# Performance work log

Hardware: AMD Instinct MI355X
Metric: run time of the kernel (lower is better)

Reference implementation:

```python
import jax, jax.numpy as jnp
import numpy as np

EPS = 1e-12  # F.normalize default eps


def setup_inputs() -> dict:
    key = jax.random.key(0)
    k1, k2, k3 = jax.random.split(key, 3)
    B, C, H, W = 4, 64, 64, 64
    background = jax.random.normal(k1, (B, C, H, W), dtype=jnp.float32)
    foreground = jax.random.normal(k2, (B, C, H, W), dtype=jnp.float32)
    # binary mask, broadcast over channels
    mask = jnp.round(jax.random.uniform(k3, (B, 1, H, W), dtype=jnp.float32))
    return {"background": background, "foreground": foreground, "mask": mask}


def _l2norm(x, axis):
    # matches torch F.normalize: x / max(||x||, eps)
    n = jnp.sqrt(jnp.sum(x * x, axis=axis, keepdims=True))
    return x / jnp.maximum(n, EPS)


def reference(background, foreground, mask):
    B, C, H, W = background.shape
    bg_flat = background.reshape(B, C, H * W)   # [B, C, K]
    fg_flat = foreground.reshape(B, C, H * W)   # [B, C, Q]
    norm_bg = _l2norm(bg_flat, axis=1)
    norm_fg = _l2norm(fg_flat, axis=1)
    # cosine-similarity scores [B, K, Q]
    attention = jnp.einsum('bck,bcq->bkq', norm_bg, norm_fg)
    attention = jax.nn.softmax(attention, axis=1)  # over bg (key) axis
    attended = jnp.einsum('bck,bkq->bcq', bg_flat, attention)
    attended = attended.reshape(B, C, H, W)
    return foreground * (1.0 - mask) + attended * mask
```

## Files before the change

kernel.cpp:

```cpp
#include <hip/hip_runtime.h>
#include <math.h>

#define CC 64
#define HWN 4096
#define QB 64
#define KSPLIT 8
#define KT 32
#define NITER (HWN / KSPLIT / KT)
#define NKC (HWN / KT)

typedef __attribute__((ext_vector_type(8))) short bf16x8;
typedef __attribute__((ext_vector_type(4))) float f32x4;

__device__ __align__(16) unsigned short g_bgT[4][HWN][CC];
__device__ __align__(16) unsigned short g_bgN[4][NKC][CC][KT];
__device__ __align__(16) unsigned short g_fgT[4][HWN][CC];

static __device__ __forceinline__ unsigned int f2bf(float x) {
  union { float f; unsigned int u; } v; v.f = x;
  return (v.u + 0x7fffu + ((v.u >> 16) & 1u)) >> 16;
}
static __device__ __forceinline__ unsigned int packbf(float lo, float hi) {
  return f2bf(lo) | (f2bf(hi) << 16);
}

__global__ __launch_bounds__(256) void prep_kernel(const float* __restrict__ bg,
                                                   const float* __restrict__ fg) {
  __shared__ float lds[64 * 65];
  const int bid = blockIdx.x;
  const int kt = bid & 63, b = (bid >> 6) & 3, which = bid >> 8;
  const float* src = (which ? fg : bg) + (size_t)b * CC * HWN + kt * 64;
  const int tid = threadIdx.x;

  {
    int c = tid >> 2, k0 = (tid & 3) * 16;
#pragma unroll
    for (int j4 = 0; j4 < 4; ++j4) {
      float4 v = *(const float4*)(src + (size_t)c * HWN + k0 + 4 * j4);
      lds[(k0 + 4 * j4 + 0) * 65 + c] = v.x;
      lds[(k0 + 4 * j4 + 1) * 65 + c] = v.y;
      lds[(k0 + 4 * j4 + 2) * 65 + c] = v.z;
      lds[(k0 + 4 * j4 + 3) * 65 + c] = v.w;
    }
  }
  __syncthreads();

  const int k = tid >> 2, u = tid & 3;
  float ss = 0.f;
#pragma unroll
  for (int j = 0; j < 16; ++j) {
    float v = lds[k * 65 + u * 16 + j];
    ss = fmaf(v, v, ss);
  }
  ss += __shfl_xor(ss, 1, 64);
  ss += __shfl_xor(ss, 2, 64);
  const float s = 1.0f / fmaxf(sqrtf(ss), 1e-12f);

  {
    unsigned int* gT32 = (unsigned int*)(which ? &g_fgT[0][0][0] : &g_bgT[0][0][0]);
    size_t R = (size_t)b * HWN + kt * 64 + k;
    unsigned int w8[8];
#pragma unroll
    for (int i = 0; i < 8; ++i) {
      int c2 = u * 16 + 2 * i;
      w8[i] = packbf(lds[k * 65 + c2] * s, lds[k * 65 + c2 + 1] * s);
    }
    *(uint4*)&gT32[R * 32 + u * 8]     = make_uint4(w8[0], w8[1], w8[2], w8[3]);
    *(uint4*)&gT32[R * 32 + u * 8 + 4] = make_uint4(w8[4], w8[5], w8[6], w8[7]);
  }

  if (which == 0) {
    unsigned int* gN32 = (unsigned int*)&g_bgN[0][0][0][0];
    int cN = tid >> 2, vN = tid & 3;
    unsigned int n8[8];
#pragma unroll
    for (int i = 0; i < 8; ++i) {
      int kk = vN * 16 + 2 * i;
      n8[i] = packbf(lds[kk * 65 + cN], lds[(kk + 1) * 65 + cN]);
    }
    int kc = kt * 2 + (vN >> 1);
    size_t RN = (((size_t)b * NKC + kc) * CC + cN) * (KT / 2) + (vN & 1) * 8;
    *(uint4*)&gN32[RN]     = make_uint4(n8[0], n8[1], n8[2], n8[3]);
    *(uint4*)&gN32[RN + 4] = make_uint4(n8[4], n8[5], n8[6], n8[7]);
  }
}

#define P_OFF 65536
#define ML_OFF 106496
#define SMEM_BYTES 108544
__global__ __launch_bounds__(512, 2) void attn_kernel(const float* __restrict__ fg,
                                                      const float* __restrict__ mask,
                                                      float* __restrict__ out) {
  __shared__ __align__(16) char smem[SMEM_BYTES];
  const int wg = blockIdx.x;
  const int wgp = (wg & 7) * 32 + (wg >> 3);
  const int b = wgp >> 6;
  const int q0 = (wgp & 63) * QB;
  const int tid = threadIdx.x;
  const int lane = tid & 63;
  const int ks = tid >> 6;
  const int m16 = lane & 15;
  const int quad = lane >> 4;

  bf16x8 Bf[4][2];
#pragma unroll
  for (int qf = 0; qf < 4; ++qf)
#pragma unroll
    for (int h = 0; h < 2; ++h)
      Bf[qf][h] = *(const bf16x8*)&g_fgT[b][q0 + qf * 16 + m16][h * 32 + quad * 8];

  const unsigned short* srcT[4];
#pragma unroll
  for (int t = 0; t < 4; ++t) {
    int uT = t * 64 + lane;
    int kk = uT >> 3, pos = uT & 7, j = pos ^ (kk & 7);
    srcT[t] = &g_bgT[b][ks * 512 + kk][j * 8];
  }

  const unsigned short* pN = &g_bgN[b][ks * 16][m16][quad * 8];

  unsigned short* P = (unsigned short*)(smem + P_OFF + ks * 5120);
  float* mL = (float*)(smem + ML_OFF);

  float l_run[4] = {0.f, 0.f, 0.f, 0.f};
  f32x4 O[4][4];
#pragma unroll
  for (int t = 0; t < 4; ++t)
#pragma unroll
    for (int qf = 0; qf < 4; ++qf) O[t][qf] = (f32x4){0.f, 0.f, 0.f, 0.f};

  char* const myT = smem + ks * 8192;

  auto stageT = [&](int bufsel) {
#pragma unroll
    for (int t = 0; t < 4; ++t) {
      __builtin_amdgcn_global_load_lds(
          (const __attribute__((address_space(1))) unsigned int*)srcT[t],
          (__attribute__((address_space(3))) unsigned int*)(myT + bufsel * 4096 + t * 1024),
          16, 0, 0);
      srcT[t] += KT * CC;
    }
  };

  bf16x8 A0r[4], A1r[4];
  auto loadN = [&](bf16x8 (&A)[4], int ch) {
#pragma unroll
    for (int t = 0; t < 4; ++t)
      A[t] = *(const bf16x8*)(pN + (size_t)ch * (CC * KT) + t * 16 * KT);
  };

  auto iter = [&](int it, int co, bf16x8 (&Ac)[4], bf16x8 (&An)[4]) {
    if (it + 1 < NITER) {
      stageT(co ^ 1);
      loadN(An, it + 1);
      asm volatile("s_waitcnt vmcnt(8)" ::: "memory");
    } else {
      asm volatile("s_waitcnt vmcnt(0)" ::: "memory");
    }

    const char* baseT = myT + co * 4096;

    f32x4 S[4][2];
    __builtin_amdgcn_s_setprio(1);
#pragma unroll
    for (int i = 0; i < 2; ++i) {
      int kk = 16 * i + m16;
      bf16x8 T0 = *(const bf16x8*)(baseT + kk * 128 + ((quad) ^ (kk & 7)) * 16);
      bf16x8 T1 = *(const bf16x8*)(baseT + kk * 128 + ((4 + quad) ^ (kk & 7)) * 16);
#pragma unroll
      for (int qf = 0; qf < 4; ++qf) {
        f32x4 acc = {0.f, 0.f, 0.f, 0.f};
        acc = __builtin_amdgcn_mfma_f32_16x16x32_bf16(T0, Bf[qf][0], acc, 0, 0, 0);
        acc = __builtin_amdgcn_mfma_f32_16x16x32_bf16(T1, Bf[qf][1], acc, 0, 0, 0);
        S[qf][i] = acc;
      }
    }
    __builtin_amdgcn_s_setprio(0);

#pragma unroll
    for (int qf = 0; qf < 4; ++qf)
#pragma unroll
      for (int i = 0; i < 2; ++i) {
        float pe[4];
#pragma unroll
        for (int r = 0; r < 4; ++r) {
          pe[r] = __expf(S[qf][i][r] - 1.0f);
          l_run[qf] += pe[r];
        }
        union { float f; unsigned int u; } x0, x1, x2, x3;
        x0.f = pe[0]; x1.f = pe[1]; x2.f = pe[2]; x3.f = pe[3];
        unsigned int p01 = __builtin_amdgcn_perm(x1.u + 0x8000u, x0.u + 0x8000u, 0x07060302u);
        unsigned int p23 = __builtin_amdgcn_perm(x3.u + 0x8000u, x2.u + 0x8000u, 0x07060302u);
        *(uint2*)&P[(qf * 16 + m16) * 40 + 16 * i + quad * 4] = make_uint2(p01, p23);
      }

    bf16x8 Pf[4];
#pragma unroll
    for (int qf = 0; qf < 4; ++qf)
      Pf[qf] = *(const bf16x8*)&P[(qf * 16 + m16) * 40 + quad * 8];
    __builtin_amdgcn_s_setprio(1);
#pragma unroll
    for (int t = 0; t < 4; ++t)
#pragma unroll
      for (int qf = 0; qf < 4; ++qf)
        O[t][qf] = __builtin_amdgcn_mfma_f32_16x16x32_bf16(Ac[t], Pf[qf], O[t][qf], 0, 0, 0);
    __builtin_amdgcn_s_setprio(0);
  };

  stageT(0);
  loadN(A0r, 0);

  for (int it2 = 0; it2 < NITER; it2 += 2) {
    iter(it2,     0, A0r, A1r);
    iter(it2 + 1, 1, A1r, A0r);
  }

#pragma unroll
  for (int qf = 0; qf < 4; ++qf) {
    l_run[qf] += __shfl_xor(l_run[qf], 16, 64);
    l_run[qf] += __shfl_xor(l_run[qf], 32, 64);
  }
  if (quad == 0) {
#pragma unroll
    for (int qf = 0; qf < 4; ++qf) mL[ks * 64 + qf * 16 + m16] = l_run[qf];
  }
  float* mO = (float*)smem;
  const float* fgB = fg + (size_t)b * CC * HWN;
  const float* mk = mask + (size_t)b * HWN;
  float* outB = out + (size_t)b * CC * HWN;

#pragma unroll
  for (int half = 0; half < 2; ++half) {
    __syncthreads();
#pragma unroll
    for (int qh = 0; qh < 2; ++qh) {
      int qf = half * 2 + qh;
#pragma unroll
      for (int t = 0; t < 4; ++t)
#pragma unroll
        for (int r = 0; r < 4; ++r)
          mO[(ks * 64 + 16 * t + quad * 4 + r) * 34 + qh * 16 + m16] = O[t][qf][r];
    }
    __syncthreads();
    {
      int q = tid & 31, cb = tid >> 5;
      int qglob = q0 + half * 32 + q;
      float L = 0.f;
#pragma unroll
      for (int s = 0; s < 8; ++s) L += mL[s * 64 + half * 32 + q];
      float invL = 1.0f / L;
      float mv = mk[qglob];
#pragma unroll
      for (int e = 0; e < 4; ++e) {
        int c = cb * 4 + e;
        float acc = 0.f;
#pragma unroll
        for (int s = 0; s < 8; ++s) acc += mO[(s * 64 + c) * 34 + q];
        float att = acc * invL;
        float fgv = fgB[(size_t)c * HWN + qglob];
        outB[(size_t)c * HWN + qglob] = fgv + mv * (att - fgv);
      }
    }
  }
}

extern "C" void kernel_launch(void* const* d_in, const int* in_sizes, int n_in,
                              void* d_out, int out_size, void* d_ws, size_t ws_size,
                              hipStream_t stream) {
  const float* background = (const float*)d_in[0];
  const float* foreground = (const float*)d_in[1];
  const float* mask       = (const float*)d_in[2];
  float* out = (float*)d_out;
  prep_kernel<<<512, 256, 0, stream>>>(background, foreground);
  attn_kernel<<<dim3(HWN / QB * 4), 512, 0, stream>>>(foreground, mask, out);
}
```

Baseline: 91.74 us.

## Keep P in registers via 16x16x16 MFMA and load bg tiles directly from global

The softmax probabilities stay in registers and are fed straight into 16x16x16 bf16 MFMAs, whose operand layout matches the score accumulator layout. This removes the LDS round trip for P. The background score tiles are now loaded from global memory into registers instead of being staged into LDS with global_load_lds, and the LDS footprint shrinks. The cost is twice as many MFMA instructions for the PV product, at half the K depth each, plus more register pressure and more outstanding global loads per iteration.

```diff
diff --git a/kernel.cpp b/kernel.cpp
--- a/kernel.cpp
+++ b/kernel.cpp
@@ -10,6 +10,7 @@
 #define NKC (HWN / KT)
 
 typedef __attribute__((ext_vector_type(8))) short bf16x8;
+typedef __attribute__((ext_vector_type(4))) short bf16x4;
 typedef __attribute__((ext_vector_type(4))) float f32x4;
 
 __device__ __align__(16) unsigned short g_bgT[4][HWN][CC];
@@ -85,9 +86,8 @@
   }
 }
 
-#define P_OFF 65536
-#define ML_OFF 106496
-#define SMEM_BYTES 108544
+#define ML_OFF 69632
+#define SMEM_BYTES 71680
 __global__ __launch_bounds__(512, 2) void attn_kernel(const float* __restrict__ fg,
                                                       const float* __restrict__ mask,
                                                       float* __restrict__ out) {
@@ -109,17 +109,9 @@
     for (int h = 0; h < 2; ++h)
       Bf[qf][h] = *(const bf16x8*)&g_fgT[b][q0 + qf * 16 + m16][h * 32 + quad * 8];
 
-  const unsigned short* srcT[4];
-#pragma unroll
-  for (int t = 0; t < 4; ++t) {
-    int uT = t * 64 + lane;
-    int kk = uT >> 3, pos = uT & 7, j = pos ^ (kk & 7);
-    srcT[t] = &g_bgT[b][ks * 512 + kk][j * 8];
-  }
-
-  const unsigned short* pN = &g_bgN[b][ks * 16][m16][quad * 8];
-
-  unsigned short* P = (unsigned short*)(smem + P_OFF + ks * 5120);
+  const unsigned short* const baseT = &g_bgT[b][ks * 512][0];
+  const unsigned short* const baseN = &g_bgN[b][ks * 16][0][0];
+
   float* mL = (float*)(smem + ML_OFF);
 
   float l_run[4] = {0.f, 0.f, 0.f, 0.f};
@@ -129,54 +121,50 @@
 #pragma unroll
     for (int qf = 0; qf < 4; ++qf) O[t][qf] = (f32x4){0.f, 0.f, 0.f, 0.f};
 
-  char* const myT = smem + ks * 8192;
-
-  auto stageT = [&](int bufsel) {
-#pragma unroll
-    for (int t = 0; t < 4; ++t) {
-      __builtin_amdgcn_global_load_lds(
-          (const __attribute__((address_space(1))) unsigned int*)srcT[t],
-          (__attribute__((address_space(3))) unsigned int*)(myT + bufsel * 4096 + t * 1024),
-          16, 0, 0);
-      srcT[t] += KT * CC;
-    }
+  auto loadT = [&](bf16x8 (&T)[2][2], int ch) {
+#pragma unroll
+    for (int i = 0; i < 2; ++i)
+#pragma unroll
+      for (int h = 0; h < 2; ++h)
+        T[i][h] = *(const bf16x8*)(baseT + (size_t)(ch * 32 + i * 16 + m16) * CC +
+                                   h * 32 + quad * 8);
   };
-
-  bf16x8 A0r[4], A1r[4];
-  auto loadN = [&](bf16x8 (&A)[4], int ch) {
-#pragma unroll
-    for (int t = 0; t < 4; ++t)
-      A[t] = *(const bf16x8*)(pN + (size_t)ch * (CC * KT) + t * 16 * KT);
+  auto loadA = [&](bf16x4 (&A)[4][2], int ch) {
+#pragma unroll
+    for (int ct = 0; ct < 4; ++ct)
+#pragma unroll
+      for (int i = 0; i < 2; ++i)
+        A[ct][i] = *(const bf16x4*)(baseN + (size_t)ch * (CC * KT) +
+                                    (ct * 16 + m16) * KT + i * 16 + quad * 4);
   };
 
-  auto iter = [&](int it, int co, bf16x8 (&Ac)[4], bf16x8 (&An)[4]) {
+  bf16x8 Ta[2][2], Tb[2][2];
+  bf16x4 Aa[4][2], Ab[4][2];
+
+  auto iter = [&](int it, bf16x8 (&T)[2][2], bf16x4 (&A)[4][2],
+                  bf16x8 (&Tn)[2][2], bf16x4 (&An)[4][2]) {
     if (it + 1 < NITER) {
-      stageT(co ^ 1);
-      loadN(An, it + 1);
-      asm volatile("s_waitcnt vmcnt(8)" ::: "memory");
+      loadT(Tn, it + 1);
+      loadA(An, it + 1);
+      asm volatile("s_waitcnt vmcnt(12)" ::: "memory");
     } else {
       asm volatile("s_waitcnt vmcnt(0)" ::: "memory");
     }
 
-    const char* baseT = myT + co * 4096;
-
     f32x4 S[4][2];
     __builtin_amdgcn_s_setprio(1);
 #pragma unroll
-    for (int i = 0; i < 2; ++i) {
-      int kk = 16 * i + m16;
-      bf16x8 T0 = *(const bf16x8*)(baseT + kk * 128 + ((quad) ^ (kk & 7)) * 16);
-      bf16x8 T1 = *(const bf16x8*)(baseT + kk * 128 + ((4 + quad) ^ (kk & 7)) * 16);
+    for (int i = 0; i < 2; ++i)
 #pragma unroll
       for (int qf = 0; qf < 4; ++qf) {
         f32x4 acc = {0.f, 0.f, 0.f, 0.f};
-        acc = __builtin_amdgcn_mfma_f32_16x16x32_bf16(T0, Bf[qf][0], acc, 0, 0, 0);
-        acc = __builtin_amdgcn_mfma_f32_16x16x32_bf16(T1, Bf[qf][1], acc, 0, 0, 0);
+        acc = __builtin_amdgcn_mfma_f32_16x16x32_bf16(T[i][0], Bf[qf][0], acc, 0, 0, 0);
+        acc = __builtin_amdgcn_mfma_f32_16x16x32_bf16(T[i][1], Bf[qf][1], acc, 0, 0, 0);
         S[qf][i] = acc;
       }
-    }
     __builtin_amdgcn_s_setprio(0);
 
+    bf16x4 Pp[4][2];
 #pragma unroll
     for (int qf = 0; qf < 4; ++qf)
 #pragma unroll
@@ -189,30 +177,31 @@
         }
         union { float f; unsigned int u; } x0, x1, x2, x3;
         x0.f = pe[0]; x1.f = pe[1]; x2.f = pe[2]; x3.f = pe[3];
-        unsigned int p01 = __builtin_amdgcn_perm(x1.u + 0x8000u, x0.u + 0x8000u, 0x07060302u);
-        unsigned int p23 = __builtin_amdgcn_perm(x3.u + 0x8000u, x2.u + 0x8000u, 0x07060302u);
-        *(uint2*)&P[(qf * 16 + m16) * 40 + 16 * i + quad * 4] = make_uint2(p01, p23);
-      }
-
-    bf16x8 Pf[4];
-#pragma unroll
-    for (int qf = 0; qf < 4; ++qf)
-      Pf[qf] = *(const bf16x8*)&P[(qf * 16 + m16) * 40 + quad * 8];
+        union { unsigned int u[2]; bf16x4 v; } pk;
+        pk.u[0] = __builtin_amdgcn_perm(x1.u + 0x8000u, x0.u + 0x8000u, 0x07060302u);
+        pk.u[1] = __builtin_amdgcn_perm(x3.u + 0x8000u, x2.u + 0x8000u, 0x07060302u);
+        Pp[qf][i] = pk.v;
+      }
+
     __builtin_amdgcn_s_setprio(1);
 #pragma unroll
-    for (int t = 0; t < 4; ++t)
-#pragma unroll
-      for (int qf = 0; qf < 4; ++qf)
-        O[t][qf] = __builtin_amdgcn_mfma_f32_16x16x32_bf16(Ac[t], Pf[qf], O[t][qf], 0, 0, 0);
+    for (int ct = 0; ct < 4; ++ct)
+#pragma unroll
+      for (int qf = 0; qf < 4; ++qf) {
+        O[ct][qf] = __builtin_amdgcn_mfma_f32_16x16x16bf16_1k(A[ct][0], Pp[qf][0],
+                                                              O[ct][qf], 0, 0, 0);
+        O[ct][qf] = __builtin_amdgcn_mfma_f32_16x16x16bf16_1k(A[ct][1], Pp[qf][1],
+                                                              O[ct][qf], 0, 0, 0);
+      }
     __builtin_amdgcn_s_setprio(0);
   };
 
-  stageT(0);
-  loadN(A0r, 0);
+  loadT(Ta, 0);
+  loadA(Aa, 0);
 
   for (int it2 = 0; it2 < NITER; it2 += 2) {
-    iter(it2,     0, A0r, A1r);
-    iter(it2 + 1, 1, A1r, A0r);
+    iter(it2,     Ta, Aa, Tb, Ab);
+    iter(it2 + 1, Tb, Ab, Ta, Aa);
   }
 
 #pragma unroll
```

Result: slower. 101.3 us (+10.4%).

## Triple-buffer bg tile LDS staging and interleave softmax with PV MFMAs

Applied to the files above, without the earlier changes.

Raises the per-wave LDS staging of the transposed background tiles from two to three buffers, prefetching two iterations ahead with adjusted vmcnt waits, so global load latency is better hidden. It also splits the softmax/P-write and PV MFMA phase into two halves so exp work on later query fragments can overlap with MFMAs on earlier ones. LDS use per block grows to about 141 KB, which with launch bounds of 2 blocks per CU may exceed LDS capacity and reduce occupancy to one block per CU.

```diff
diff --git a/kernel.cpp b/kernel.cpp
--- a/kernel.cpp
+++ b/kernel.cpp
@@ -85,9 +85,9 @@
   }
 }
 
-#define P_OFF 65536
-#define ML_OFF 106496
-#define SMEM_BYTES 108544
+#define P_OFF 98304
+#define ML_OFF 139264
+#define SMEM_BYTES 141312
 __global__ __launch_bounds__(512, 2) void attn_kernel(const float* __restrict__ fg,
                                                       const float* __restrict__ mask,
                                                       float* __restrict__ out) {
@@ -129,14 +129,14 @@
 #pragma unroll
     for (int qf = 0; qf < 4; ++qf) O[t][qf] = (f32x4){0.f, 0.f, 0.f, 0.f};
 
-  char* const myT = smem + ks * 8192;
-
-  auto stageT = [&](int bufsel) {
+  char* const myT = smem + ks * 12288;
+
+  auto stageT = [&](int bufoff) {
 #pragma unroll
     for (int t = 0; t < 4; ++t) {
       __builtin_amdgcn_global_load_lds(
           (const __attribute__((address_space(1))) unsigned int*)srcT[t],
-          (__attribute__((address_space(3))) unsigned int*)(myT + bufsel * 4096 + t * 1024),
+          (__attribute__((address_space(3))) unsigned int*)(myT + bufoff + t * 1024),
           16, 0, 0);
       srcT[t] += KT * CC;
     }
@@ -149,16 +149,37 @@
       A[t] = *(const bf16x8*)(pN + (size_t)ch * (CC * KT) + t * 16 * KT);
   };
 
-  auto iter = [&](int it, int co, bf16x8 (&Ac)[4], bf16x8 (&An)[4]) {
-    if (it + 1 < NITER) {
-      stageT(co ^ 1);
-      loadN(An, it + 1);
+  auto softmaxQ = [&](const f32x4 (&S)[4][2], int qf) {
+#pragma unroll
+    for (int i = 0; i < 2; ++i) {
+      float pe[4];
+#pragma unroll
+      for (int r = 0; r < 4; ++r) {
+        pe[r] = __expf(S[qf][i][r] - 1.0f);
+        l_run[qf] += pe[r];
+      }
+      union { float f; unsigned int u; } x0, x1, x2, x3;
+      x0.f = pe[0]; x1.f = pe[1]; x2.f = pe[2]; x3.f = pe[3];
+      unsigned int p01 = __builtin_amdgcn_perm(x1.u + 0x8000u, x0.u + 0x8000u, 0x07060302u);
+      unsigned int p23 = __builtin_amdgcn_perm(x3.u + 0x8000u, x2.u + 0x8000u, 0x07060302u);
+      *(uint2*)&P[(qf * 16 + m16) * 40 + 16 * i + quad * 4] = make_uint2(p01, p23);
+    }
+  };
+
+  int sA = 0, sB = 4096, sC = 8192;
+
+  auto iter = [&](int it, bf16x8 (&Ac)[4], bf16x8 (&An)[4]) {
+    if (it + 1 < NITER) loadN(An, it + 1);
+    if (it + 2 < NITER) {
+      stageT(sC);
+      asm volatile("s_waitcnt vmcnt(12)" ::: "memory");
+    } else if (it + 1 < NITER) {
       asm volatile("s_waitcnt vmcnt(8)" ::: "memory");
     } else {
       asm volatile("s_waitcnt vmcnt(0)" ::: "memory");
     }
 
-    const char* baseT = myT + co * 4096;
+    const char* baseT = myT + sA;
 
     f32x4 S[4][2];
     __builtin_amdgcn_s_setprio(1);
@@ -177,42 +198,43 @@
     }
     __builtin_amdgcn_s_setprio(0);
 
-#pragma unroll
-    for (int qf = 0; qf < 4; ++qf)
-#pragma unroll
-      for (int i = 0; i < 2; ++i) {
-        float pe[4];
-#pragma unroll
-        for (int r = 0; r < 4; ++r) {
-          pe[r] = __expf(S[qf][i][r] - 1.0f);
-          l_run[qf] += pe[r];
-        }
-        union { float f; unsigned int u; } x0, x1, x2, x3;
-        x0.f = pe[0]; x1.f = pe[1]; x2.f = pe[2]; x3.f = pe[3];
-        unsigned int p01 = __builtin_amdgcn_perm(x1.u + 0x8000u, x0.u + 0x8000u, 0x07060302u);
-        unsigned int p23 = __builtin_amdgcn_perm(x3.u + 0x8000u, x2.u + 0x8000u, 0x07060302u);
-        *(uint2*)&P[(qf * 16 + m16) * 40 + 16 * i + quad * 4] = make_uint2(p01, p23);
-      }
-
-    bf16x8 Pf[4];
-#pragma unroll
-    for (int qf = 0; qf < 4; ++qf)
-      Pf[qf] = *(const bf16x8*)&P[(qf * 16 + m16) * 40 + quad * 8];
-    __builtin_amdgcn_s_setprio(1);
-#pragma unroll
-    for (int t = 0; t < 4; ++t)
-#pragma unroll
-      for (int qf = 0; qf < 4; ++qf)
-        O[t][qf] = __builtin_amdgcn_mfma_f32_16x16x32_bf16(Ac[t], Pf[qf], O[t][qf], 0, 0, 0);
-    __builtin_amdgcn_s_setprio(0);
-  };
-
-  stageT(0);
+    softmaxQ(S, 0);
+    softmaxQ(S, 1);
+    {
+      bf16x8 Pf0 = *(const bf16x8*)&P[(0 * 16 + m16) * 40 + quad * 8];
+      bf16x8 Pf1 = *(const bf16x8*)&P[(1 * 16 + m16) * 40 + quad * 8];
+      __builtin_amdgcn_s_setprio(1);
+#pragma unroll
+      for (int t = 0; t < 4; ++t) {
+        O[t][0] = __builtin_amdgcn_mfma_f32_16x16x32_bf16(Ac[t], Pf0, O[t][0], 0, 0, 0);
+        O[t][1] = __builtin_amdgcn_mfma_f32_16x16x32_bf16(Ac[t], Pf1, O[t][1], 0, 0, 0);
+      }
+      __builtin_amdgcn_s_setprio(0);
+    }
+    softmaxQ(S, 2);
+    softmaxQ(S, 3);
+    {
+      bf16x8 Pf2 = *(const bf16x8*)&P[(2 * 16 + m16) * 40 + quad * 8];
+      bf16x8 Pf3 = *(const bf16x8*)&P[(3 * 16 + m16) * 40 + quad * 8];
+      __builtin_amdgcn_s_setprio(1);
+#pragma unroll
+      for (int t = 0; t < 4; ++t) {
+        O[t][2] = __builtin_amdgcn_mfma_f32_16x16x32_bf16(Ac[t], Pf2, O[t][2], 0, 0, 0);
+        O[t][3] = __builtin_amdgcn_mfma_f32_16x16x32_bf16(Ac[t], Pf3, O[t][3], 0, 0, 0);
+      }
+      __builtin_amdgcn_s_setprio(0);
+    }
+
+    int tmp = sA; sA = sB; sB = sC; sC = tmp;
+  };
+
+  stageT(sA);
   loadN(A0r, 0);
+  stageT(sB);
 
   for (int it2 = 0; it2 < NITER; it2 += 2) {
-    iter(it2,     0, A0r, A1r);
-    iter(it2 + 1, 1, A1r, A0r);
+    iter(it2,     A0r, A1r);
+    iter(it2 + 1, A1r, A0r);
   }
 
 #pragma unroll
```

Result: slower. 93.59 us (+2.0%).
